# Performance work log

Hardware: AMD Instinct MI355X
Metric: run time of the kernel (lower is better)

Reference implementation:

```python
import jax, jax.numpy as jnp
import numpy as np

H = 8          # num_heads
D = 64         # out_dims = input_dims / num_heads
DM = H * D     # input_dims = 512
B, S = 2, 2048


def _linear(x, W, b):
    # torch nn.Linear: x @ W.T + b, W: [out, in]
    return jnp.einsum('...d,ed->...e', x, W) + b


def setup_inputs() -> dict:
    key = jax.random.key(0)
    ks = jax.random.split(key, 12)
    inp = {
        'query': jax.random.normal(ks[0], (B, S, DM), dtype=jnp.float32),
        'key': jax.random.normal(ks[1], (B, S, DM), dtype=jnp.float32),
        'value': jax.random.normal(ks[2], (B, S, DM), dtype=jnp.float32),
        'Wq': jax.random.normal(ks[3], (D, D), dtype=jnp.float32) * 0.02,
        'bq': jnp.zeros((D,), dtype=jnp.float32),
        'Wk': jax.random.normal(ks[4], (D, D), dtype=jnp.float32) * 0.02,
        'bk': jnp.zeros((D,), dtype=jnp.float32),
        'Wv': jax.random.normal(ks[5], (D, D), dtype=jnp.float32) * 0.02,
        'bv': jnp.zeros((D,), dtype=jnp.float32),
        'Wo': jax.random.normal(ks[6], (DM, DM), dtype=jnp.float32) * 0.02,
        'bo': jnp.zeros((DM,), dtype=jnp.float32),
        'mask': jax.random.randint(ks[7], (B, 1, 1, S), 0, 2, dtype=jnp.int32),
    }
    return inp


def reference(query, key, value, Wq, bq, Wk, bk, Wv, bv, Wo, bo, mask):
    b, qlen = query.shape[0], query.shape[1]
    klen = key.shape[1]
    # split heads: [B, S, H, D]
    q = _linear(query.reshape(b, qlen, H, D), Wq, bq)
    k = _linear(key.reshape(b, klen, H, D), Wk, bk)
    v = _linear(value.reshape(b, klen, H, D), Wv, bv)
    # scores: [B, H, Q, K]
    attn = jnp.einsum('bqhd,bkhd->bhqk', q, k)
    attn = jnp.where(mask == 0, jnp.float32(-1e20), attn)
    # NOTE: original scale is num_heads ** 1 / 2 == H / 2 (Python precedence quirk)
    score = jax.nn.softmax(attn * (2.0 / H), axis=-1)
    # out einsum gives [B, Q, D, H]; flattening gives (d, h) feature order
    out = jnp.einsum('bhqv,bvhd->bqdh', score, v)
    out = out.reshape(b, qlen, D * H)
    return _linear(out, Wo, bo)
```

## Files before the change

kernel.cpp:

```cpp
#include <hip/hip_runtime.h>
#include <math.h>

typedef float f32x4 __attribute__((ext_vector_type(4)));
typedef short s16x8 __attribute__((ext_vector_type(8)));
typedef unsigned short ushort_t;

namespace {
constexpr int kH  = 8;
constexpr int kD  = 64;
constexpr int kDM = 512;
constexpr int kB  = 2;
constexpr int kS  = 2048;
constexpr size_t kNE = (size_t)kB * kS * kDM;
constexpr size_t kNL = (size_t)kB * kH * kS;
}

__device__ __forceinline__ void split_bf16(float x, ushort_t& hi, ushort_t& lo) {
  union { float f; unsigned u; } a; a.f = x;
  hi = (ushort_t)(a.u >> 16);
  union { unsigned u; float f; } hh; hh.u = a.u & 0xffff0000u;
  union { float f; unsigned u; } r; r.f = x - hh.f;
  lo = (ushort_t)(r.u >> 16);
}
__device__ __forceinline__ ushort_t rne_bf16(float x) {
  union { float f; unsigned u; } a; a.f = x;
  const unsigned t = a.u + 0x7fffu + ((a.u >> 16) & 1u);
  return (ushort_t)(t >> 16);
}
__device__ __forceinline__ float bf_to_f(unsigned u16) {
  union { unsigned u; float f; } a; a.u = u16 << 16; return a.f;
}

__global__ __launch_bounds__(256, 2)
void kv_proj_kernel(const float* __restrict__ xk, const float* __restrict__ xv,
                    const float* __restrict__ Wk, const float* __restrict__ bk,
                    const float* __restrict__ Wv, const float* __restrict__ bv,
                    const float* __restrict__ Wo, const float* __restrict__ Wq,
                    ushort_t* __restrict__ wo_h, ushort_t* __restrict__ wo_l,
                    ushort_t* __restrict__ wq_h, ushort_t* __restrict__ wq_l,
                    ushort_t* __restrict__ k_hi, ushort_t* __restrict__ vt_hi) {
  const int which = blockIdx.z;
  if (which == 2) {
    const int bid = blockIdx.y * 64 + blockIdx.x;
    if (bid < 128) {
      const int gi = (bid * 256 + threadIdx.x) * 8;
      const int e  = gi >> 9;
      const int g0 = gi & 511;
      const int fbase = (g0 & 63) * 8 + (g0 >> 6);
      ushort_t h8[8], l8[8];
      #pragma unroll
      for (int j = 0; j < 8; ++j)
        split_bf16(Wo[(size_t)e * kDM + fbase + j * 8], h8[j], l8[j]);
      int4 hp, lp;
      hp.x = (int)((unsigned)h8[0] | ((unsigned)h8[1] << 16));
      hp.y = (int)((unsigned)h8[2] | ((unsigned)h8[3] << 16));
      hp.z = (int)((unsigned)h8[4] | ((unsigned)h8[5] << 16));
      hp.w = (int)((unsigned)h8[6] | ((unsigned)h8[7] << 16));
      lp.x = (int)((unsigned)l8[0] | ((unsigned)l8[1] << 16));
      lp.y = (int)((unsigned)l8[2] | ((unsigned)l8[3] << 16));
      lp.z = (int)((unsigned)l8[4] | ((unsigned)l8[5] << 16));
      lp.w = (int)((unsigned)l8[6] | ((unsigned)l8[7] << 16));
      *(int4*)&wo_h[(size_t)e * kDM + g0] = hp;
      *(int4*)&wo_l[(size_t)e * kDM + g0] = lp;
    } else if (bid == 128) {
      #pragma unroll
      for (int cc = 0; cc < 4; ++cc) {
        const int i = (cc * 256 + threadIdx.x) * 4;
        const float4 v = *(const float4*)&Wq[i];
        ushort_t h4[4], l4[4];
        split_bf16(v.x, h4[0], l4[0]);
        split_bf16(v.y, h4[1], l4[1]);
        split_bf16(v.z, h4[2], l4[2]);
        split_bf16(v.w, h4[3], l4[3]);
        int2 hp, lp;
        hp.x = (int)((unsigned)h4[0] | ((unsigned)h4[1] << 16));
        hp.y = (int)((unsigned)h4[2] | ((unsigned)h4[3] << 16));
        lp.x = (int)((unsigned)l4[0] | ((unsigned)l4[1] << 16));
        lp.y = (int)((unsigned)l4[2] | ((unsigned)l4[3] << 16));
        *(int2*)&wq_h[i] = hp;
        *(int2*)&wq_l[i] = lp;
      }
    }
    return;
  }

  __shared__ __align__(16) ushort_t Xh[64][72];
  __shared__ __align__(16) ushort_t Xl[64][72];
  const float* x = which ? xv : xk;
  const float* W = which ? Wv : Wk;
  const float* bias = which ? bv : bk;
  const int h = blockIdx.y;
  const int t0g = blockIdx.x * 64;
  const int b = t0g >> 11, s0 = t0g & (kS - 1);
  const int tid  = threadIdx.x;
  const int w    = tid >> 6;
  const int lane = tid & 63;
  const int ln   = lane & 15;
  const int quad = lane >> 4;
  const size_t hb = ((size_t)b * kH + h) * (size_t)(kS * kD);

  #pragma unroll
  for (int cc = 0; cc < 4; ++cc) {
    const int id = tid + cc * 256;
    const int r = id >> 4, c = id & 15;
    const float4 v = *(const float4*)&x[((size_t)t0g + r) * kDM + h * kD + c * 4];
    ushort_t hh[4], ll[4];
    split_bf16(v.x, hh[0], ll[0]);
    split_bf16(v.y, hh[1], ll[1]);
    split_bf16(v.z, hh[2], ll[2]);
    split_bf16(v.w, hh[3], ll[3]);
    int2 hp, lp;
    hp.x = (int)((unsigned)hh[0] | ((unsigned)hh[1] << 16));
    hp.y = (int)((unsigned)hh[2] | ((unsigned)hh[3] << 16));
    lp.x = (int)((unsigned)ll[0] | ((unsigned)ll[1] << 16));
    lp.y = (int)((unsigned)ll[2] | ((unsigned)ll[3] << 16));
    *(int2*)&Xh[r][c * 4] = hp;
    *(int2*)&Xl[r][c * 4] = lp;
  }
  __syncthreads();

  f32x4 C[4];
  #pragma unroll
  for (int eb = 0; eb < 4; ++eb) C[eb] = (f32x4){0.f, 0.f, 0.f, 0.f};
  #pragma unroll
  for (int kc = 0; kc < 2; ++kc) {
    const s16x8 ah = *(const s16x8*)&Xh[w * 16 + ln][kc * 32 + quad * 8];
    const s16x8 al = *(const s16x8*)&Xl[w * 16 + ln][kc * 32 + quad * 8];
    #pragma unroll
    for (int eb = 0; eb < 4; ++eb) {
      const float* wp = &W[(size_t)(eb * 16 + ln) * kD + kc * 32 + quad * 8];
      const float4 w0 = *(const float4*)wp;
      const float4 w1 = *(const float4*)(wp + 4);
      const float ws[8] = {w0.x, w0.y, w0.z, w0.w, w1.x, w1.y, w1.z, w1.w};
      s16x8 bh, bl;
      #pragma unroll
      for (int j = 0; j < 8; ++j) {
        ushort_t hi, lo;
        split_bf16(ws[j], hi, lo);
        bh[j] = (short)hi; bl[j] = (short)lo;
      }
      C[eb] = __builtin_amdgcn_mfma_f32_16x16x32_bf16(ah, bh, C[eb], 0, 0, 0);
      C[eb] = __builtin_amdgcn_mfma_f32_16x16x32_bf16(ah, bl, C[eb], 0, 0, 0);
      C[eb] = __builtin_amdgcn_mfma_f32_16x16x32_bf16(al, bh, C[eb], 0, 0, 0);
    }
  }
  __syncthreads();

  if (which == 0) {
    #pragma unroll
    for (int eb = 0; eb < 4; ++eb) {
      const float be = bias[eb * 16 + ln];
      #pragma unroll
      for (int r = 0; r < 4; ++r)
        Xh[w * 16 + quad * 4 + r][eb * 16 + ln] = rne_bf16(C[eb][r] + be);
    }
    __syncthreads();
    #pragma unroll
    for (int cc = 0; cc < 2; ++cc) {
      const int id = tid + cc * 256;
      const int r = id >> 3, c = id & 7;
      *(int4*)&k_hi[hb + (size_t)(s0 + r) * kD + c * 8] = *(int4*)&Xh[r][c * 8];
    }
  } else {
    #pragma unroll
    for (int eb = 0; eb < 4; ++eb) {
      const float be = bias[eb * 16 + ln];
      #pragma unroll
      for (int r = 0; r < 4; ++r)
        Xh[eb * 16 + ln][w * 16 + quad * 4 + r] = rne_bf16(C[eb][r] + be);
    }
    __syncthreads();
    #pragma unroll
    for (int cc = 0; cc < 2; ++cc) {
      const int id = tid + cc * 256;
      const int r = id >> 3, c = id & 7;
      *(int4*)&vt_hi[hb + (size_t)r * kS + s0 + c * 8] = *(int4*)&Xh[r][c * 8];
    }
  }
}

__global__ __launch_bounds__(256, 4)
void attn_kernel(const float* __restrict__ xq,
                 const ushort_t* __restrict__ wq_h, const ushort_t* __restrict__ wq_l,
                 const float* __restrict__ bq,
                 const ushort_t* __restrict__ k_hi, const ushort_t* __restrict__ vt_hi,
                 const int* __restrict__ mask,
                 ushort_t* __restrict__ Opart, float* __restrict__ lws) {
  __shared__ __align__(16) ushort_t smem[128 * 72];
  __shared__ __align__(16) ushort_t Pbm[4 * 32 * 40];
  __shared__ float Mz[64];
  ushort_t (*QT)[72] = (ushort_t(*)[72])smem;
  ushort_t (*Kh)[72] = (ushort_t(*)[72])smem;
  ushort_t (*Vh)[72] = (ushort_t(*)[72])(smem + 64 * 72);
  ushort_t (*Pb)[32][40] = (ushort_t(*)[32][40])Pbm;

  const int tid  = threadIdx.x;
  const int w    = tid >> 6;
  const int lane = tid & 63;
  const int ln   = lane & 15;
  const int quad = lane >> 4;
  const int h    = blockIdx.y;
  const int b    = blockIdx.z >> 2;
  const int quarter = blockIdx.z & 3;
  const int q0   = blockIdx.x * 128;
  const size_t hb = ((size_t)b * kH + h) * (size_t)(kS * kD);

  s16x8 aqh[2][2];
  #pragma unroll
  for (int g = 0; g < 2; ++g) {
    const int qrow = q0 + w * 32 + g * 16 + ln;
    f32x4 C[4];
    #pragma unroll
    for (int eb = 0; eb < 4; ++eb) C[eb] = (f32x4){0.f, 0.f, 0.f, 0.f};
    #pragma unroll
    for (int kc = 0; kc < 2; ++kc) {
      const float* xp = &xq[((size_t)b * kS + qrow) * kDM + h * kD + kc * 32 + quad * 8];
      const float4 x0 = *(const float4*)xp;
      const float4 x1 = *(const float4*)(xp + 4);
      const float xs[8] = {x0.x, x0.y, x0.z, x0.w, x1.x, x1.y, x1.z, x1.w};
      s16x8 ah, al;
      #pragma unroll
      for (int j = 0; j < 8; ++j) {
        ushort_t hi, lo;
        split_bf16(xs[j], hi, lo);
        ah[j] = (short)hi; al[j] = (short)lo;
      }
      #pragma unroll
      for (int eb = 0; eb < 4; ++eb) {
        const s16x8 bh = *(const s16x8*)&wq_h[(size_t)(eb * 16 + ln) * kD + kc * 32 + quad * 8];
        const s16x8 bl = *(const s16x8*)&wq_l[(size_t)(eb * 16 + ln) * kD + kc * 32 + quad * 8];
        C[eb] = __builtin_amdgcn_mfma_f32_16x16x32_bf16(ah, bh, C[eb], 0, 0, 0);
        C[eb] = __builtin_amdgcn_mfma_f32_16x16x32_bf16(ah, bl, C[eb], 0, 0, 0);
        C[eb] = __builtin_amdgcn_mfma_f32_16x16x32_bf16(al, bh, C[eb], 0, 0, 0);
      }
    }
    #pragma unroll
    for (int eb = 0; eb < 4; ++eb) {
      const float be = bq[eb * 16 + ln];
      #pragma unroll
      for (int r = 0; r < 4; ++r)
        QT[w * 32 + g * 16 + quad * 4 + r][eb * 16 + ln] = rne_bf16(C[eb][r] + be);
    }
    #pragma unroll
    for (int db = 0; db < 2; ++db)
      aqh[g][db] = *(const s16x8*)&QT[w * 32 + g * 16 + ln][db * 32 + quad * 8];
  }
  __syncthreads();

  f32x4 O[2][4];
  #pragma unroll
  for (int g = 0; g < 2; ++g)
    #pragma unroll
    for (int db = 0; db < 4; ++db) O[g][db] = (f32x4){0.f, 0.f, 0.f, 0.f};
  float rs[2][4] = {};

  const int kt0 = quarter * 8;
  for (int kt = kt0; kt < kt0 + 8; ++kt) {
    __syncthreads();
    {
      const ushort_t* gkh = k_hi + hb + (size_t)kt * 64 * kD;
      const ushort_t* gvh = vt_hi + hb + (size_t)kt * 64;
      #pragma unroll
      for (int cc = 0; cc < 2; ++cc) {
        const int id = tid + cc * 256;
        const int r = id >> 3, c = id & 7;
        *(int4*)&Kh[r][c * 8] = *(const int4*)&gkh[r * kD + c * 8];
        *(int4*)&Vh[r][c * 8] = *(const int4*)&gvh[(size_t)r * kS + c * 8];
      }
      if (tid < 64) Mz[tid] = (mask[(size_t)b * kS + kt * 64 + tid] != 0) ? 1.0f : 0.0f;
    }
    __syncthreads();

    #pragma unroll
    for (int h32 = 0; h32 < 2; ++h32) {
      f32x4 C[2][2];
      #pragma unroll
      for (int g = 0; g < 2; ++g) {
        C[g][0] = (f32x4){0.f, 0.f, 0.f, 0.f};
        C[g][1] = (f32x4){0.f, 0.f, 0.f, 0.f};
      }
      #pragma unroll
      for (int db = 0; db < 2; ++db) {
        const s16x8 bh0 = *(const s16x8*)&Kh[h32 * 32 + ln][db * 32 + quad * 8];
        const s16x8 bh1 = *(const s16x8*)&Kh[h32 * 32 + 16 + ln][db * 32 + quad * 8];
        #pragma unroll
        for (int g = 0; g < 2; ++g) {
          C[g][0] = __builtin_amdgcn_mfma_f32_16x16x32_bf16(aqh[g][db], bh0, C[g][0], 0, 0, 0);
          C[g][1] = __builtin_amdgcn_mfma_f32_16x16x32_bf16(aqh[g][db], bh1, C[g][1], 0, 0, 0);
        }
      }
      #pragma unroll
      for (int g = 0; g < 2; ++g) {
        #pragma unroll
        for (int kb = 0; kb < 2; ++kb) {
          const float mz = Mz[h32 * 32 + kb * 16 + ln];
          #pragma unroll
          for (int r = 0; r < 4; ++r) {
            const float p = mz * __expf(0.25f * C[g][kb][r]);
            union { float f; unsigned u; } pa; pa.f = p;
            const unsigned t = pa.u + 0x7fffu + ((pa.u >> 16) & 1u);
            Pb[w][g * 16 + quad * 4 + r][kb * 16 + ln] = (ushort_t)(t >> 16);
            union { unsigned u; float f; } pr; pr.u = t & 0xffff0000u;
            rs[g][r] += pr.f;
          }
        }
      }
      {
        const s16x8 ph0 = *(const s16x8*)&Pb[w][ln][quad * 8];
        const s16x8 ph1 = *(const s16x8*)&Pb[w][16 + ln][quad * 8];
        #pragma unroll
        for (int db = 0; db < 4; ++db) {
          const s16x8 vh = *(const s16x8*)&Vh[db * 16 + ln][h32 * 32 + quad * 8];
          O[0][db] = __builtin_amdgcn_mfma_f32_16x16x32_bf16(ph0, vh, O[0][db], 0, 0, 0);
          O[1][db] = __builtin_amdgcn_mfma_f32_16x16x32_bf16(ph1, vh, O[1][db], 0, 0, 0);
        }
      }
    }
  }

  #pragma unroll
  for (int m = 1; m < 16; m <<= 1) {
    #pragma unroll
    for (int g = 0; g < 2; ++g)
      #pragma unroll
      for (int r = 0; r < 4; ++r) rs[g][r] += __shfl_xor(rs[g][r], m);
  }
  if (ln == 0) {
    #pragma unroll
    for (int g = 0; g < 2; ++g) {
      float* lp = lws + (size_t)quarter * kNL + ((size_t)b * kH + h) * kS +
                  q0 + w * 32 + g * 16 + quad * 4;
      #pragma unroll
      for (int r = 0; r < 4; ++r) lp[r] = rs[g][r];
    }
  }

  __syncthreads();
  #pragma unroll
  for (int g = 0; g < 2; ++g)
    #pragma unroll
    for (int db = 0; db < 4; ++db)
      #pragma unroll
      for (int r = 0; r < 4; ++r)
        QT[w * 32 + g * 16 + quad * 4 + r][db * 16 + ln] = rne_bf16(O[g][db][r]);
  __syncthreads();
  ushort_t* op = Opart + (size_t)quarter * kNE;
  #pragma unroll
  for (int cc = 0; cc < 4; ++cc) {
    const int id = tid + cc * 256;
    const int r = id >> 3, c = id & 7;
    *(int4*)&op[((size_t)b * kS + q0 + r) * kDM + h * kD + c * 8] = *(int4*)&QT[r][c * 8];
  }
}

__global__ __launch_bounds__(256, 2)
void out_proj_kernel(const ushort_t* __restrict__ Opart, const float* __restrict__ lws,
                     const ushort_t* __restrict__ wh, const ushort_t* __restrict__ wl,
                     const float* __restrict__ bo, float* __restrict__ out) {
  __shared__ __align__(16) ushort_t Ah[32][40];
  __shared__ __align__(16) ushort_t Al[32][40];
  __shared__ __align__(16) ushort_t Bh[128][40];
  __shared__ __align__(16) ushort_t Bl[128][40];
  __shared__ float linv[kH][32];
  const int t0 = blockIdx.x * 32;
  const int e0 = blockIdx.y * 128;
  const int b  = t0 >> 11;
  const int s0 = t0 & (kS - 1);
  const int tid  = threadIdx.x;
  const int w    = tid >> 6;
  const int lane = tid & 63;
  const int ln   = lane & 15;
  const int quad = lane >> 4;
  const int tsub = w & 1;
  const int esub = w >> 1;

  {
    const int hh = tid >> 5, r = tid & 31;
    const size_t base = ((size_t)b * kH + hh) * kS + s0 + r;
    linv[hh][r] = 1.0f / (lws[base] + lws[kNL + base] +
                          lws[2 * kNL + base] + lws[3 * kNL + base]);
  }

  f32x4 C[4];
  #pragma unroll
  for (int eb = 0; eb < 4; ++eb) C[eb] = (f32x4){0.f, 0.f, 0.f, 0.f};

  for (int k0 = 0; k0 < kDM; k0 += 32) {
    __syncthreads();
    const int hh = k0 >> 6;
    {
      const int r = tid >> 3, c4 = (tid & 7) * 4;
      const size_t off = (size_t)(t0 + r) * kDM + k0 + c4;
      float a0 = 0.f, a1 = 0.f, a2 = 0.f, a3 = 0.f;
      #pragma unroll
      for (int q = 0; q < 4; ++q) {
        const int2 u = *(const int2*)&Opart[(size_t)q * kNE + off];
        a0 += bf_to_f((unsigned)u.x & 0xffffu);
        a1 += bf_to_f((unsigned)u.x >> 16);
        a2 += bf_to_f((unsigned)u.y & 0xffffu);
        a3 += bf_to_f((unsigned)u.y >> 16);
      }
      const float li = linv[hh][r];
      a0 *= li; a1 *= li; a2 *= li; a3 *= li;
      ushort_t h4[4], l4[4];
      split_bf16(a0, h4[0], l4[0]);
      split_bf16(a1, h4[1], l4[1]);
      split_bf16(a2, h4[2], l4[2]);
      split_bf16(a3, h4[3], l4[3]);
      int2 hp, lp;
      hp.x = (int)((unsigned)h4[0] | ((unsigned)h4[1] << 16));
      hp.y = (int)((unsigned)h4[2] | ((unsigned)h4[3] << 16));
      lp.x = (int)((unsigned)l4[0] | ((unsigned)l4[1] << 16));
      lp.y = (int)((unsigned)l4[2] | ((unsigned)l4[3] << 16));
      *(int2*)&Ah[r][c4] = hp;
      *(int2*)&Al[r][c4] = lp;
    }
    #pragma unroll
    for (int cc = 0; cc < 2; ++cc) {
      const int id = tid + cc * 256;
      const int r = id >> 2, c = (id & 3) * 8;
      *(int4*)&Bh[r][c] = *(const int4*)&wh[(size_t)(e0 + r) * kDM + k0 + c];
      *(int4*)&Bl[r][c] = *(const int4*)&wl[(size_t)(e0 + r) * kDM + k0 + c];
    }
    __syncthreads();
    const s16x8 ah = *(const s16x8*)&Ah[tsub * 16 + ln][quad * 8];
    const s16x8 al = *(const s16x8*)&Al[tsub * 16 + ln][quad * 8];
    #pragma unroll
    for (int eb = 0; eb < 4; ++eb) {
      const s16x8 bh = *(const s16x8*)&Bh[esub * 64 + eb * 16 + ln][quad * 8];
      const s16x8 bl = *(const s16x8*)&Bl[esub * 64 + eb * 16 + ln][quad * 8];
      C[eb] = __builtin_amdgcn_mfma_f32_16x16x32_bf16(ah, bh, C[eb], 0, 0, 0);
      C[eb] = __builtin_amdgcn_mfma_f32_16x16x32_bf16(ah, bl, C[eb], 0, 0, 0);
      C[eb] = __builtin_amdgcn_mfma_f32_16x16x32_bf16(al, bh, C[eb], 0, 0, 0);
    }
  }

  #pragma unroll
  for (int eb = 0; eb < 4; ++eb) {
    const int e = e0 + esub * 64 + eb * 16 + ln;
    const float be = bo[e];
    #pragma unroll
    for (int r = 0; r < 4; ++r) {
      const int t = t0 + tsub * 16 + quad * 4 + r;
      out[(size_t)t * kDM + e] = C[eb][r] + be;
    }
  }
}

extern "C" void kernel_launch(void* const* d_in, const int* in_sizes, int n_in,
                              void* d_out, int out_size, void* d_ws, size_t ws_size,
                              hipStream_t stream) {
  const float* query = (const float*)d_in[0];
  const float* key   = (const float*)d_in[1];
  const float* value = (const float*)d_in[2];
  const float* Wq = (const float*)d_in[3];
  const float* bq = (const float*)d_in[4];
  const float* Wk = (const float*)d_in[5];
  const float* bk = (const float*)d_in[6];
  const float* Wv = (const float*)d_in[7];
  const float* bv = (const float*)d_in[8];
  const float* Wo = (const float*)d_in[9];
  const float* bo = (const float*)d_in[10];
  const int* mask = (const int*)d_in[11];
  float* out = (float*)d_out;

  ushort_t* k_hi  = (ushort_t*)d_ws;
  ushort_t* vt_hi = k_hi + kNE;
  ushort_t* wo_h  = vt_hi + kNE;
  ushort_t* wo_l  = wo_h + (size_t)kDM * kDM;
  ushort_t* Opart = wo_l + (size_t)kDM * kDM;
  float*    lws   = (float*)(Opart + 4 * kNE);
  ushort_t* wq_h  = (ushort_t*)(lws + 4 * kNL);
  ushort_t* wq_l  = wq_h + kD * kD;

  kv_proj_kernel<<<dim3(kB * kS / 64, kH, 3), 256, 0, stream>>>(
      key, value, Wk, bk, Wv, bv, Wo, Wq, wo_h, wo_l, wq_h, wq_l, k_hi, vt_hi);
  attn_kernel<<<dim3(kS / 128, kH, kB * 4), 256, 0, stream>>>(
      query, wq_h, wq_l, bq, k_hi, vt_hi, mask, Opart, lws);
  out_proj_kernel<<<dim3(kB * kS / 32, kDM / 128), 256, 0, stream>>>(
      Opart, lws, wo_h, wo_l, bo, out);
}
```

Baseline: 170.7 us.

## Prefetch next K/V tile into registers during attention compute

The attention kernel's K/V tile loop now loads the next tile's K, V and mask values from global memory into registers while the current tile is being computed. It then writes them to LDS at the top of the next iteration, so global-load latency overlaps with MFMA work. The redundant barrier after the Q projection is removed, since the loop's first barrier covers it. The kv_proj kernel's launch bounds are also raised to 4 blocks per CU, which may cap its register use and cause spills.

```diff
diff --git a/kernel.cpp b/kernel.cpp
--- a/kernel.cpp
+++ b/kernel.cpp
@@ -31,7 +31,7 @@
   union { unsigned u; float f; } a; a.u = u16 << 16; return a.f;
 }
 
-__global__ __launch_bounds__(256, 2)
+__global__ __launch_bounds__(256, 4)
 void kv_proj_kernel(const float* __restrict__ xk, const float* __restrict__ xv,
                     const float* __restrict__ Wk, const float* __restrict__ bk,
                     const float* __restrict__ Wv, const float* __restrict__ bv,
@@ -205,6 +205,9 @@
   const int q0   = blockIdx.x * 128;
   const size_t hb = ((size_t)b * kH + h) * (size_t)(kS * kD);
 
+  const int sr = tid >> 3;
+  const int sc = (tid & 7) * 8;
+
   s16x8 aqh[2][2];
   #pragma unroll
   for (int g = 0; g < 2; ++g) {
@@ -245,7 +248,6 @@
     for (int db = 0; db < 2; ++db)
       aqh[g][db] = *(const s16x8*)&QT[w * 32 + g * 16 + ln][db * 32 + quad * 8];
   }
-  __syncthreads();
 
   f32x4 O[2][4];
   #pragma unroll
@@ -255,21 +257,43 @@
   float rs[2][4] = {};
 
   const int kt0 = quarter * 8;
-  for (int kt = kt0; kt < kt0 + 8; ++kt) {
+  int4 kr[2], vr[2];
+  int mload = 0;
+  {
+    const ushort_t* gkh = k_hi + hb + (size_t)kt0 * 64 * kD;
+    const ushort_t* gvh = vt_hi + hb + (size_t)kt0 * 64;
+    #pragma unroll
+    for (int cc = 0; cc < 2; ++cc) {
+      const int r = sr + cc * 32;
+      kr[cc] = *(const int4*)&gkh[r * kD + sc];
+      vr[cc] = *(const int4*)&gvh[(size_t)r * kS + sc];
+    }
+    if (tid < 64) mload = mask[(size_t)b * kS + kt0 * 64 + tid];
+  }
+
+  for (int i = 0; i < 8; ++i) {
     __syncthreads();
-    {
-      const ushort_t* gkh = k_hi + hb + (size_t)kt * 64 * kD;
-      const ushort_t* gvh = vt_hi + hb + (size_t)kt * 64;
+    #pragma unroll
+    for (int cc = 0; cc < 2; ++cc) {
+      const int r = sr + cc * 32;
+      *(int4*)&Kh[r][sc] = kr[cc];
+      *(int4*)&Vh[r][sc] = vr[cc];
+    }
+    if (tid < 64) Mz[tid] = (mload != 0) ? 1.0f : 0.0f;
+    __syncthreads();
+
+    if (i < 7) {
+      const int ktn = kt0 + i + 1;
+      const ushort_t* gkh = k_hi + hb + (size_t)ktn * 64 * kD;
+      const ushort_t* gvh = vt_hi + hb + (size_t)ktn * 64;
       #pragma unroll
       for (int cc = 0; cc < 2; ++cc) {
-        const int id = tid + cc * 256;
-        const int r = id >> 3, c = id & 7;
-        *(int4*)&Kh[r][c * 8] = *(const int4*)&gkh[r * kD + c * 8];
-        *(int4*)&Vh[r][c * 8] = *(const int4*)&gvh[(size_t)r * kS + c * 8];
-      }
-      if (tid < 64) Mz[tid] = (mask[(size_t)b * kS + kt * 64 + tid] != 0) ? 1.0f : 0.0f;
-    }
-    __syncthreads();
+        const int r = sr + cc * 32;
+        kr[cc] = *(const int4*)&gkh[r * kD + sc];
+        vr[cc] = *(const int4*)&gvh[(size_t)r * kS + sc];
+      }
+      if (tid < 64) mload = mask[(size_t)b * kS + ktn * 64 + tid];
+    }
 
     #pragma unroll
     for (int h32 = 0; h32 < 2; ++h32) {
```

Measured after the change: 186.4 us. +9.2%, slower.
